# Kernel optimization log

Measured on AMD Instinct MI355X. Metric: run time of the kernel, lower is better.

Reference implementation:

```python
import jax, jax.numpy as jnp
import numpy as np

TANH_EPS = 1e-06
LOG2PI = float(np.log(2.0 * np.pi))


def _atanh(x):
    x = jnp.clip(x, -1.0 + TANH_EPS, 1.0 - TANH_EPS)
    return 0.5 * (jnp.log1p(x) - jnp.log1p(-x))


def setup_inputs() -> dict:
    key = jax.random.key(0)
    ks = jax.random.split(key, 12)
    T, B, O, H, A = 256, 1024, 128, 128, 8
    s = 0.05
    return {
        "obs_seq": jax.random.normal(ks[0], (T, B, O), jnp.float32),
        "actions_seq": jax.random.uniform(ks[1], (T, B, A), jnp.float32, -0.99, 0.99),
        "dones_seq": (jax.random.uniform(ks[2], (T, B)) < 0.02).astype(jnp.float32),
        "h0": jnp.zeros((B, H), jnp.float32),
        "c0": jnp.zeros((B, H), jnp.float32),
        "enc_w1": s * jax.random.normal(ks[3], (H, O), jnp.float32),
        "enc_b1": jnp.zeros((H,), jnp.float32),
        "enc_w2": s * jax.random.normal(ks[4], (H, H), jnp.float32),
        "enc_b2": jnp.zeros((H,), jnp.float32),
        "w_ih": s * jax.random.normal(ks[5], (4 * H, H), jnp.float32),
        "w_hh": s * jax.random.normal(ks[6], (4 * H, H), jnp.float32),
        "b_ih": jnp.zeros((4 * H,), jnp.float32),
        "b_hh": jnp.zeros((4 * H,), jnp.float32),
        "am_w": 0.01 * jax.random.normal(ks[7], (A, H), jnp.float32),
        "am_b": jnp.zeros((A,), jnp.float32),
        "actor_logstd": jnp.zeros((A,), jnp.float32),
        "cr_w": s * jax.random.normal(ks[8], (1, H), jnp.float32),
        "cr_b": jnp.zeros((1,), jnp.float32),
    }


def reference(obs_seq, actions_seq, dones_seq, h0, c0,
              enc_w1, enc_b1, enc_w2, enc_b2,
              w_ih, w_hh, b_ih, b_hh,
              am_w, am_b, actor_logstd, cr_w, cr_b):
    # Encoder (batched over all timesteps): two tanh MLP layers.
    x = jnp.tanh(jnp.einsum('tbo,ho->tbh', obs_seq, enc_w1) + enc_b1)
    x = jnp.tanh(jnp.einsum('tbh,gh->tbg', x, enc_w2) + enc_b2)
    # Precompute input contribution to gates: [T, B, 4H]
    xg = jnp.einsum('tbh,gh->tbg', x, w_ih) + b_ih

    def step(carry, inp):
        h, c = carry
        xg_t, d_t = inp
        m = (1.0 - d_t)[:, None]  # done-masking reset
        h = h * m
        c = c * m
        g = xg_t + h @ w_hh.T + b_hh
        i, f, gg, o = jnp.split(g, 4, axis=-1)
        c2 = jax.nn.sigmoid(f) * c + jax.nn.sigmoid(i) * jnp.tanh(gg)
        h2 = jax.nn.sigmoid(o) * jnp.tanh(c2)
        return (h2, c2), h2

    (hT, cT), ys = jax.lax.scan(step, (h0, c0), (xg, dones_seq))  # ys: [T, B, H]

    values = (jnp.einsum('tbh,vh->tbv', ys, cr_w) + cr_b)[..., 0]  # [T, B]
    mean = jnp.einsum('tbh,ah->tba', ys, am_w) + am_b  # [T, B, A]
    logstd = actor_logstd  # [A]
    u = _atanh(actions_seq)
    # Normal log-prob per dim, summed over action dims
    z = (u - mean) * jnp.exp(-logstd)
    lp_gauss = jnp.sum(-0.5 * z * z - logstd - 0.5 * LOG2PI, axis=-1)
    log_jac = jnp.sum(jnp.log(1.0 - actions_seq ** 2 + TANH_EPS), axis=-1)
    logprobs = lp_gauss - log_jac
    entropies = jnp.sum(0.5 + 0.5 * LOG2PI + logstd) + log_jac
    return logprobs, entropies, values, hT, cT
```

## Files before the change

### kernel.cpp

```cpp
#include <hip/hip_runtime.h>

typedef float f32x4 __attribute__((ext_vector_type(4)));
typedef short short8 __attribute__((ext_vector_type(8)));
typedef short s16x4 __attribute__((ext_vector_type(4)));

#define MFMA16(a, b, c) __builtin_amdgcn_mfma_f32_16x16x32_bf16((a), (b), (c), 0, 0, 0)

#define T_ 256
#define B_ 1024
#define H_ 128
#define TB_ 262144
#define BH_ 131072
#define LOG2PI_F 1.8378770664093453f

__device__ inline short f2bf(float f) {
    unsigned u = __builtin_bit_cast(unsigned, f);
    u += 0x7fffu + ((u >> 16) & 1u);
    return (short)(u >> 16);
}
__device__ inline float fexp(float x) { return __builtin_amdgcn_exp2f(x * 1.4426950408889634f); }
__device__ inline float fsigm(float x) { return __builtin_amdgcn_rcpf(1.f + fexp(-x)); }
__device__ inline float ftanh(float x) { return 1.f - 2.f * __builtin_amdgcn_rcpf(fexp(2.f * x) + 1.f); }

__device__ inline short8 pack8(float4 u0, float4 u1) {
    short8 p;
    p[0] = f2bf(u0.x); p[1] = f2bf(u0.y); p[2] = f2bf(u0.z); p[3] = f2bf(u0.w);
    p[4] = f2bf(u1.x); p[5] = f2bf(u1.y); p[6] = f2bf(u1.z); p[7] = f2bf(u1.w);
    return p;
}

__global__ __launch_bounds__(512, 4) void ex_kernel(
    const float* __restrict__ obs, const float* __restrict__ eb1,
    const float* __restrict__ eb2,
    const float* __restrict__ w1f, const float* __restrict__ w2f,
    short* __restrict__ x2p)
{
    __shared__ __align__(16) short xtA[64 * 128];
    __shared__ __align__(16) short xtB[64 * 128];
    __shared__ __align__(16) short xtC[64 * 128];
    const int tid = threadIdx.x;
    const int l = tid & 63, w = tid >> 6;
    const int l15 = l & 15, kg = l >> 4;
    const int srow = tid >> 3, sln = tid & 7;
    const int ssw = (srow & 7) << 3;

    short8 fw1[4], fw2[4];
#pragma unroll
    for (int kk = 0; kk < 4; ++kk) {
        const float* s1 = w1f + (w * 16 + l15) * 128 + kk * 32 + 8 * kg;
        const float* s2 = w2f + (w * 16 + l15) * 128 + kk * 32 + 8 * kg;
        fw1[kk] = pack8(*(const float4*)s1, *(const float4*)(s1 + 4));
        fw2[kk] = pack8(*(const float4*)s2, *(const float4*)(s2 + 4));
        asm volatile("" : "+v"(fw1[kk]), "+v"(fw2[kk]));
    }
    const float bb1 = eb1[w * 16 + l15], bb2 = eb2[w * 16 + l15];

    const int NT = 8;
    const int t0 = blockIdx.x * NT;

    {
        const float* src = obs + ((size_t)t0 * 64 + srow) * 128 + sln * 16;
#pragma unroll
        for (int ii = 0; ii < 2; ++ii) {
            float4 v0 = *(const float4*)(src + ii * 8);
            float4 v1 = *(const float4*)(src + ii * 8 + 4);
            *(short8*)(xtA + srow * 128 + ((sln * 16 + ii * 8) ^ ssw)) = pack8(v0, v1);
        }
    }
    __syncthreads();

    for (int i = 0; i < NT; ++i) {
        const int tile = t0 + i;
        short* bufO = (i & 1) ? xtB : xtA;
        short* bufN = (i & 1) ? xtA : xtB;

        float4 pf[4];
        {
            const int tn = (i + 1 < NT) ? tile + 1 : tile;
            const float* src = obs + ((size_t)tn * 64 + srow) * 128 + sln * 16;
#pragma unroll
            for (int ii = 0; ii < 4; ++ii) pf[ii] = *(const float4*)(src + ii * 4);
        }

#pragma unroll
        for (int mf = 0; mf < 4; ++mf) {
            const int ra = mf * 16 + l15, swa = (ra & 7) << 3;
            short8 a[4];
#pragma unroll
            for (int kk = 0; kk < 4; ++kk)
                a[kk] = *(const short8*)&bufO[ra * 128 + ((kk * 32 + 8 * kg) ^ swa)];
            f32x4 acc = {bb1, bb1, bb1, bb1};
#pragma unroll
            for (int kk = 0; kk < 4; ++kk) acc = MFMA16(a[kk], fw1[kk], acc);
#pragma unroll
            for (int j = 0; j < 4; ++j) {
                int rw = mf * 16 + kg * 4 + j;
                xtC[rw * 128 + ((w * 16 + l15) ^ ((rw & 7) << 3))] = f2bf(ftanh(acc[j]));
            }
        }
        __syncthreads();

        const int t = (tile * 64) >> 10;
        const int b_base = (tile * 64) & 1023;
#pragma unroll
        for (int mf = 0; mf < 4; ++mf) {
            const int ra = mf * 16 + l15, swa = (ra & 7) << 3;
            short8 a[4];
#pragma unroll
            for (int kk = 0; kk < 4; ++kk)
                a[kk] = *(const short8*)&xtC[ra * 128 + ((kk * 32 + 8 * kg) ^ swa)];
            f32x4 acc = {bb2, bb2, bb2, bb2};
#pragma unroll
            for (int kk = 0; kk < 4; ++kk) acc = MFMA16(a[kk], fw2[kk], acc);
#pragma unroll
            for (int j = 0; j < 4; ++j) {
                int b = b_base + mf * 16 + kg * 4 + j;
                size_t idx = (((size_t)t * 256 + (b >> 2)) * 4 + (b & 3)) * 128 + w * 16 + l15;
                x2p[idx] = f2bf(ftanh(acc[j]));
            }
        }
#pragma unroll
        for (int ii = 0; ii < 2; ++ii) {
            *(short8*)(bufN + srow * 128 + ((sln * 16 + ii * 8) ^ ssw)) =
                pack8(pf[ii * 2], pf[ii * 2 + 1]);
        }
        __syncthreads();
    }
}

__global__ __launch_bounds__(512) void lstm_kernel(
    const short* __restrict__ x2p, const float* __restrict__ whh,
    const float* __restrict__ wih,
    const float* __restrict__ h0, const float* __restrict__ c0,
    const float* __restrict__ bhh, const float* __restrict__ bih,
    const float* __restrict__ dones,
    const float* __restrict__ amw, const float* __restrict__ crw,
    const float* __restrict__ amb, const float* __restrict__ crb,
    float* __restrict__ headbuf, float* __restrict__ out)
{
    __shared__ __align__(16) short hbuf[2][4 * 160];
    __shared__ __align__(16) short hring[16 * 640];
    __shared__ __align__(16) short x2b[2][16 * 160];
    __shared__ float dlds[1028];
    const int tid = threadIdx.x;
    const int l = tid & 63, w = tid >> 6;
    const int l15 = l & 15, kg = l >> 4;
    const int b0 = blockIdx.x * 4;
    const int d = w * 16 + l15;
    const int blk = blockIdx.x;
    const int xsw = (l15 & 7) << 3;

    short8 bfr[4][4], bfi[4][4];
#pragma unroll
    for (int s = 0; s < 4; ++s)
#pragma unroll
        for (int kk = 0; kk < 4; ++kk) {
            const float* sr = whh + ((s * 128 + d) * 128 + kk * 32 + 8 * kg);
            const float* si = wih + ((s * 128 + d) * 128 + kk * 32 + 8 * kg);
            bfr[s][kk] = pack8(*(const float4*)sr, *(const float4*)(sr + 4));
            bfi[s][kk] = pack8(*(const float4*)si, *(const float4*)(si + 4));
            asm volatile("" : "+v"(bfr[s][kk]), "+v"(bfi[s][kk]));
        }

    short8 hb4[4];
#pragma unroll
    for (int kk = 0; kk < 4; ++kk) {
        if (l15 == 0) {
            const float* s0 = crw + kk * 32 + 8 * kg;
            hb4[kk] = pack8(*(const float4*)s0, *(const float4*)(s0 + 4));
        } else if (l15 <= 8) {
            const float* s0 = amw + (l15 - 1) * 128 + kk * 32 + 8 * kg;
            hb4[kk] = pack8(*(const float4*)s0, *(const float4*)(s0 + 4));
        } else {
            hb4[kk] = short8{0, 0, 0, 0, 0, 0, 0, 0};
        }
        asm volatile("" : "+v"(hb4[kk]));
    }
    const float biasH = (l15 == 0) ? crb[0] : (l15 <= 8 ? amb[l15 - 1] : 0.f);

    for (int i = tid; i < 1028; i += 512) {
        int t = i >> 2, jj = i & 3;
        dlds[i] = (t < 256) ? 1.f - dones[t * 1024 + b0 + jj] : 1.f;
    }

    float bh[4];
#pragma unroll
    for (int s = 0; s < 4; ++s) bh[s] = bhh[s * 128 + d] + bih[s * 128 + d];

    const int st_toff = tid >> 7, st_j = (tid >> 5) & 3, st_dim = (tid & 31) * 4;
    const int st_row = st_j * 4 + st_toff;
    const int xrow160 = st_row * 160 + (st_dim ^ ((st_row & 7) << 3));
#define X2GIDX(G) ((((size_t)(((G) * 4 + st_toff) <= 255 ? ((G) * 4 + st_toff) : 255) * 256 + blk) * 4 + st_j) * 128 + st_dim)

    {
        s16x4 v0 = *(const s16x4*)(x2p + X2GIDX(0));
        s16x4 v1 = *(const s16x4*)(x2p + X2GIDX(1));
        *(s16x4*)&x2b[0][xrow160] = v0;
        *(s16x4*)&x2b[1][xrow160] = v1;
    }
    s16x4 xpf = *(const s16x4*)(x2p + X2GIDX(2));
    asm volatile("s_waitcnt lgkmcnt(0)" ::: "memory");
    __syncthreads();

    f32x4 xgA[4], xgB[4];
#pragma unroll
    for (int s = 0; s < 4; ++s) {
        short8 ax[4];
#pragma unroll
        for (int kk = 0; kk < 4; ++kk)
            ax[kk] = *(const short8*)&x2b[0][l15 * 160 + ((kk * 32 + kg * 8) ^ xsw)];
        f32x4 accX = {bh[s], bh[s], bh[s], bh[s]};
#pragma unroll
        for (int kk = 0; kk < 4; ++kk) accX = MFMA16(ax[kk], bfi[s][kk], accX);
        xgA[s] = accX;
    }

    float h = h0[(b0 + kg) * 128 + d];
    float c = c0[(b0 + kg) * 128 + d];
    hbuf[0][kg * 160 + d] = f2bf(h * dlds[kg]);
    asm volatile("s_waitcnt lgkmcnt(0)" ::: "memory");
    __syncthreads();

    const int aoff = (l15 >> 2) * 160;
    float mreg = dlds[kg];

#define LSTM_STEP(t, hb, i_s, xgC, xgN, x2R, DO_T3, GNEXT, DO_HEAD)                        \
    {                                                                                      \
        short8 a[4];                                                                       \
        _Pragma("unroll")                                                                  \
        for (int kk = 0; kk < 4; ++kk)                                                     \
            a[kk] = *(const short8*)&hbuf[hb][aoff + kk * 32 + kg * 8];                    \
        f32x4 acc[4];                                                                      \
        _Pragma("unroll")                                                                  \
        for (int s = 0; s < 4; ++s) acc[s] = xgC[s];                                       \
        _Pragma("unroll")                                                                  \
        for (int kk = 0; kk < 4; ++kk)                                                     \
            _Pragma("unroll")                                                              \
            for (int s = 0; s < 4; ++s) acc[s] = MFMA16(a[kk], bfr[s][kk], acc[s]);        \
        {           \
            short8 ax[4];                                                                  \
            _Pragma("unroll")                                                              \
            for (int kk = 0; kk < 4; ++kk)                                                 \
                ax[kk] = *(const short8*)&x2R[l15 * 160 + ((kk * 32 + kg * 8) ^ xsw)];     \
            f32x4 accX = {bh[i_s], bh[i_s], bh[i_s], bh[i_s]};                             \
            _Pragma("unroll")                                                              \
            for (int kk = 0; kk < 4; ++kk) accX = MFMA16(ax[kk], bfi[i_s][kk], accX);      \
            xgN[i_s] = accX;                                                               \
        }                                                                                  \
        if (DO_HEAD) {                 \
            int th = (t) - 8 + w;                                                          \
            const short* hr = &hring[(th & 15) * 640];                                     \
            short8 ah[4];                                                                  \
            _Pragma("unroll")                                                              \
            for (int kk = 0; kk < 4; ++kk)                                                 \
                ah[kk] = *(const short8*)&hr[aoff + kk * 32 + kg * 8];                     \
            f32x4 aH = {biasH, biasH, biasH, biasH};                                       \
            _Pragma("unroll")                                                              \
            for (int kk = 0; kk < 4; ++kk) aH = MFMA16(ah[kk], hb4[kk], aH);               \
            if (l15 < 9) headbuf[(th * 1024 + b0 + kg) * 12 + l15] = aH[0];                \
        }                                                                                  \
        if (DO_T3) {                                                                      \
            *(s16x4*)&x2W[xrow160] = xpf;                                                  \
            xpf = *(const s16x4*)(x2p + X2GIDX(GNEXT));                                    \
        }                                                                                  \
        float mn = dlds[((t) + 1) * 4 + kg];                                               \
        float gi = acc[0][i_s];                                                            \
        float gf = acc[1][i_s];                                                            \
        float gg = acc[2][i_s];                                                            \
        float go = acc[3][i_s];                                                            \
        c = fsigm(gf) * (c * mreg) + fsigm(gi) * ftanh(gg);                                \
        float h2 = fsigm(go) * ftanh(c);                                                   \
        h = h2;                                                                            \
        mreg = mn;                                                                         \
        hbuf[(hb) ^ 1][kg * 160 + d] = f2bf(h2 * mn);                                      \
        hring[((t) & 15) * 640 + kg * 160 + d] = f2bf(h2);                                 \
        asm volatile("s_waitcnt lgkmcnt(0)" ::: "memory");                                 \
        __builtin_amdgcn_s_barrier();                                                      \
        asm volatile("" ::: "memory");                                                     \
    }

    for (int g = 0; g < 64; g += 2) {
        {
            const int tb = g * 4;
            const short* x2R = &x2b[1][0];
            short* x2W = &x2b[0][0];
            LSTM_STEP(tb + 0, 0, 0, xgA, xgB, x2R, 0, 0, (g > 0));
            LSTM_STEP(tb + 1, 1, 1, xgA, xgB, x2R, 0, 0, 0);
            LSTM_STEP(tb + 2, 0, 2, xgA, xgB, x2R, 0, 0, 0);
            LSTM_STEP(tb + 3, 1, 3, xgA, xgB, x2R, 1, (g + 3), 0);
        }
        {
            const int tb = (g + 1) * 4;
            const short* x2R = &x2b[0][0];
            short* x2W = &x2b[1][0];
            LSTM_STEP(tb + 0, 0, 0, xgB, xgA, x2R, 0, 0, 0);
            LSTM_STEP(tb + 1, 1, 1, xgB, xgA, x2R, 0, 0, 0);
            LSTM_STEP(tb + 2, 0, 2, xgB, xgA, x2R, 0, 0, 0);
            LSTM_STEP(tb + 3, 1, 3, xgB, xgA, x2R, 1, (g + 4), 0);
        }
    }
#undef LSTM_STEP
#undef X2GIDX

    {
        int th = 248 + w;
        const short* hr = &hring[(th & 15) * 640];
        short8 ah[4];
#pragma unroll
        for (int kk = 0; kk < 4; ++kk)
            ah[kk] = *(const short8*)&hr[aoff + kk * 32 + kg * 8];
        f32x4 aH = {biasH, biasH, biasH, biasH};
#pragma unroll
        for (int kk = 0; kk < 4; ++kk) aH = MFMA16(ah[kk], hb4[kk], aH);
        if (l15 < 9) headbuf[(th * 1024 + b0 + kg) * 12 + l15] = aH[0];
    }

    out[3 * TB_ + (b0 + kg) * 128 + d] = h;
    out[3 * TB_ + BH_ + (b0 + kg) * 128 + d] = c;
}

__global__ __launch_bounds__(256) void headepi_kernel(
    const float* __restrict__ headbuf, const float* __restrict__ lstd,
    const float* __restrict__ actions, float* __restrict__ out)
{
    const int r = blockIdx.x * 256 + threadIdx.x;
    const float* hp = headbuf + (size_t)r * 12;
    float4 m0 = *(const float4*)(hp);
    float4 m1 = *(const float4*)(hp + 4);
    float4 m2 = *(const float4*)(hp + 8);
    const float* ap = actions + (size_t)r * 8;
    float4 a0 = *(const float4*)(ap);
    float4 a1 = *(const float4*)(ap + 4);
    float mean[8] = {m0.y, m0.z, m0.w, m1.x, m1.y, m1.z, m1.w, m2.x};
    float act[8] = {a0.x, a0.y, a0.z, a0.w, a1.x, a1.y, a1.z, a1.w};
    float lp = 0.f, lj = 0.f, entS = 0.f;
#pragma unroll
    for (int ai = 0; ai < 8; ++ai) {
        float x = act[ai];
        float xc = fminf(fmaxf(x, -1.f + 1e-6f), 1.f - 1e-6f);
        float u = 0.5f * logf((1.f + xc) / (1.f - xc));
        float ls = lstd[ai];
        float z = (u - mean[ai]) * expf(-ls);
        lp += -0.5f * z * z - ls;
        lj += logf(1.f - x * x + 1e-6f);
        entS += ls;
    }
    lp -= 8.f * 0.5f * LOG2PI_F;
    entS += 8.f * (0.5f + 0.5f * LOG2PI_F);
    out[r] = lp - lj;
    out[TB_ + r] = entS + lj;
    out[2 * TB_ + r] = m0.x;
}

extern "C" void kernel_launch(void* const* d_in, const int* in_sizes, int n_in,
                              void* d_out, int out_size, void* d_ws, size_t ws_size,
                              hipStream_t stream) {
    const float* obs   = (const float*)d_in[0];
    const float* acts  = (const float*)d_in[1];
    const float* dones = (const float*)d_in[2];
    const float* h0    = (const float*)d_in[3];
    const float* c0    = (const float*)d_in[4];
    const float* w1    = (const float*)d_in[5];
    const float* b1    = (const float*)d_in[6];
    const float* w2    = (const float*)d_in[7];
    const float* b2    = (const float*)d_in[8];
    const float* wih   = (const float*)d_in[9];
    const float* whh   = (const float*)d_in[10];
    const float* bih   = (const float*)d_in[11];
    const float* bhh   = (const float*)d_in[12];
    const float* amw   = (const float*)d_in[13];
    const float* amb   = (const float*)d_in[14];
    const float* lstd  = (const float*)d_in[15];
    const float* crw   = (const float*)d_in[16];
    const float* crb   = (const float*)d_in[17];
    float* out = (float*)d_out;

    char* ws = (char*)d_ws;
    short* x2p = (short*)(ws);
    float* hbf = (float*)(ws + 67108864);
    if (ws_size < (size_t)67108864 + 12582912) return;

    hipLaunchKernelGGL(ex_kernel, dim3(512), dim3(512), 0, stream,
                       obs, b1, b2, w1, w2, x2p);
    hipLaunchKernelGGL(lstm_kernel, dim3(256), dim3(512), 0, stream,
                       x2p, whh, wih, h0, c0, bhh, bih, dones, amw, crw, amb, crb, hbf, out);
    hipLaunchKernelGGL(headepi_kernel, dim3(1024), dim3(256), 0, stream,
                       hbf, lstd, acts, out);
}
```

Baseline: 216.2 us.

## Fuse observation encoder into recurrent LSTM kernel, dropping the separate encoder pass

The two-layer tanh encoder no longer runs as its own kernel. Each LSTM block now loads obs for its 4 batch rows, runs both encoder layers with weights held in LDS, and spreads that work across the per-step schedule (stage obs, layer 1, layer 2 on separate steps). This removes the separate launch and the bf16 x2 round trip through global memory. In exchange each step of the latency-bound recurrent loop carries extra LDS traffic and MFMA work, the head computation is offset by a different step lag, and LDS use grows by 64KB of encoder weights per block.

```diff
diff --git a/kernel.cpp b/kernel.cpp
--- a/kernel.cpp
+++ b/kernel.cpp
@@ -29,126 +29,66 @@
     return p;
 }
 
-__global__ __launch_bounds__(512, 4) void ex_kernel(
-    const float* __restrict__ obs, const float* __restrict__ eb1,
-    const float* __restrict__ eb2,
-    const float* __restrict__ w1f, const float* __restrict__ w2f,
-    short* __restrict__ x2p)
+__device__ __forceinline__ void enc_layer(
+    const short* inb, const short* wL, float bias, short* outb,
+    int l15, int kg, int w)
 {
-    __shared__ __align__(16) short xtA[64 * 128];
-    __shared__ __align__(16) short xtB[64 * 128];
-    __shared__ __align__(16) short xtC[64 * 128];
-    const int tid = threadIdx.x;
-    const int l = tid & 63, w = tid >> 6;
-    const int l15 = l & 15, kg = l >> 4;
-    const int srow = tid >> 3, sln = tid & 7;
-    const int ssw = (srow & 7) << 3;
-
-    short8 fw1[4], fw2[4];
+    const int xsw = (l15 & 7) << 3;
+    const int wr = w * 16 + l15, wsw = (wr & 7) << 3;
+    short8 a[4], b[4];
 #pragma unroll
     for (int kk = 0; kk < 4; ++kk) {
-        const float* s1 = w1f + (w * 16 + l15) * 128 + kk * 32 + 8 * kg;
-        const float* s2 = w2f + (w * 16 + l15) * 128 + kk * 32 + 8 * kg;
-        fw1[kk] = pack8(*(const float4*)s1, *(const float4*)(s1 + 4));
-        fw2[kk] = pack8(*(const float4*)s2, *(const float4*)(s2 + 4));
-        asm volatile("" : "+v"(fw1[kk]), "+v"(fw2[kk]));
-    }
-    const float bb1 = eb1[w * 16 + l15], bb2 = eb2[w * 16 + l15];
-
-    const int NT = 8;
-    const int t0 = blockIdx.x * NT;
-
-    {
-        const float* src = obs + ((size_t)t0 * 64 + srow) * 128 + sln * 16;
-#pragma unroll
-        for (int ii = 0; ii < 2; ++ii) {
-            float4 v0 = *(const float4*)(src + ii * 8);
-            float4 v1 = *(const float4*)(src + ii * 8 + 4);
-            *(short8*)(xtA + srow * 128 + ((sln * 16 + ii * 8) ^ ssw)) = pack8(v0, v1);
-        }
-    }
-    __syncthreads();
-
-    for (int i = 0; i < NT; ++i) {
-        const int tile = t0 + i;
-        short* bufO = (i & 1) ? xtB : xtA;
-        short* bufN = (i & 1) ? xtA : xtB;
-
-        float4 pf[4];
-        {
-            const int tn = (i + 1 < NT) ? tile + 1 : tile;
-            const float* src = obs + ((size_t)tn * 64 + srow) * 128 + sln * 16;
-#pragma unroll
-            for (int ii = 0; ii < 4; ++ii) pf[ii] = *(const float4*)(src + ii * 4);
-        }
-
-#pragma unroll
-        for (int mf = 0; mf < 4; ++mf) {
-            const int ra = mf * 16 + l15, swa = (ra & 7) << 3;
-            short8 a[4];
-#pragma unroll
-            for (int kk = 0; kk < 4; ++kk)
-                a[kk] = *(const short8*)&bufO[ra * 128 + ((kk * 32 + 8 * kg) ^ swa)];
-            f32x4 acc = {bb1, bb1, bb1, bb1};
-#pragma unroll
-            for (int kk = 0; kk < 4; ++kk) acc = MFMA16(a[kk], fw1[kk], acc);
-#pragma unroll
-            for (int j = 0; j < 4; ++j) {
-                int rw = mf * 16 + kg * 4 + j;
-                xtC[rw * 128 + ((w * 16 + l15) ^ ((rw & 7) << 3))] = f2bf(ftanh(acc[j]));
-            }
-        }
-        __syncthreads();
-
-        const int t = (tile * 64) >> 10;
-        const int b_base = (tile * 64) & 1023;
-#pragma unroll
-        for (int mf = 0; mf < 4; ++mf) {
-            const int ra = mf * 16 + l15, swa = (ra & 7) << 3;
-            short8 a[4];
-#pragma unroll
-            for (int kk = 0; kk < 4; ++kk)
-                a[kk] = *(const short8*)&xtC[ra * 128 + ((kk * 32 + 8 * kg) ^ swa)];
-            f32x4 acc = {bb2, bb2, bb2, bb2};
-#pragma unroll
-            for (int kk = 0; kk < 4; ++kk) acc = MFMA16(a[kk], fw2[kk], acc);
-#pragma unroll
-            for (int j = 0; j < 4; ++j) {
-                int b = b_base + mf * 16 + kg * 4 + j;
-                size_t idx = (((size_t)t * 256 + (b >> 2)) * 4 + (b & 3)) * 128 + w * 16 + l15;
-                x2p[idx] = f2bf(ftanh(acc[j]));
-            }
-        }
-#pragma unroll
-        for (int ii = 0; ii < 2; ++ii) {
-            *(short8*)(bufN + srow * 128 + ((sln * 16 + ii * 8) ^ ssw)) =
-                pack8(pf[ii * 2], pf[ii * 2 + 1]);
-        }
-        __syncthreads();
+        a[kk] = *(const short8*)&inb[l15 * 160 + ((kk * 32 + kg * 8) ^ xsw)];
+        b[kk] = *(const short8*)&wL[wr * 128 + ((kk * 32 + kg * 8) ^ wsw)];
+    }
+    f32x4 acc = {bias, bias, bias, bias};
+#pragma unroll
+    for (int kk = 0; kk < 4; ++kk) acc = MFMA16(a[kk], b[kk], acc);
+#pragma unroll
+    for (int j = 0; j < 4; ++j) {
+        const int row = kg * 4 + j;
+        outb[row * 160 + (wr ^ ((row & 7) << 3))] = f2bf(ftanh(acc[j]));
     }
 }
 
 __global__ __launch_bounds__(512) void lstm_kernel(
-    const short* __restrict__ x2p, const float* __restrict__ whh,
-    const float* __restrict__ wih,
+    const float* __restrict__ obs,
+    const float* __restrict__ whh, const float* __restrict__ wih,
     const float* __restrict__ h0, const float* __restrict__ c0,
     const float* __restrict__ bhh, const float* __restrict__ bih,
     const float* __restrict__ dones,
     const float* __restrict__ amw, const float* __restrict__ crw,
     const float* __restrict__ amb, const float* __restrict__ crb,
+    const float* __restrict__ w1f, const float* __restrict__ eb1,
+    const float* __restrict__ w2f, const float* __restrict__ eb2,
     float* __restrict__ headbuf, float* __restrict__ out)
 {
+    __shared__ __align__(16) short w1L[128 * 128];
+    __shared__ __align__(16) short w2L[128 * 128];
+    __shared__ __align__(16) short obsb[16 * 160];
+    __shared__ __align__(16) short x1b[16 * 160];
+    __shared__ __align__(16) short x2b[2][16 * 160];
     __shared__ __align__(16) short hbuf[2][4 * 160];
     __shared__ __align__(16) short hring[16 * 640];
-    __shared__ __align__(16) short x2b[2][16 * 160];
     __shared__ float dlds[1028];
     const int tid = threadIdx.x;
     const int l = tid & 63, w = tid >> 6;
     const int l15 = l & 15, kg = l >> 4;
     const int b0 = blockIdx.x * 4;
     const int d = w * 16 + l15;
-    const int blk = blockIdx.x;
     const int xsw = (l15 & 7) << 3;
+
+    for (int idx = tid * 4; idx < 16384; idx += 2048) {
+        const int row = idx >> 7, db = idx & 127;
+        float4 v1 = *(const float4*)(w1f + idx);
+        float4 v2 = *(const float4*)(w2f + idx);
+        s16x4 p1, p2;
+        p1[0] = f2bf(v1.x); p1[1] = f2bf(v1.y); p1[2] = f2bf(v1.z); p1[3] = f2bf(v1.w);
+        p2[0] = f2bf(v2.x); p2[1] = f2bf(v2.y); p2[2] = f2bf(v2.z); p2[3] = f2bf(v2.w);
+        const int sa = row * 128 + (db ^ ((row & 7) << 3));
+        *(s16x4*)&w1L[sa] = p1;
+        *(s16x4*)&w2L[sa] = p2;
+    }
 
     short8 bfr[4][4], bfi[4][4];
 #pragma unroll
@@ -177,6 +117,7 @@
         asm volatile("" : "+v"(hb4[kk]));
     }
     const float biasH = (l15 == 0) ? crb[0] : (l15 <= 8 ? amb[l15 - 1] : 0.f);
+    const float bb1 = eb1[d], bb2 = eb2[d];
 
     for (int i = tid; i < 1028; i += 512) {
         int t = i >> 2, jj = i & 3;
@@ -187,20 +128,36 @@
 #pragma unroll
     for (int s = 0; s < 4; ++s) bh[s] = bhh[s * 128 + d] + bih[s * 128 + d];
 
-    const int st_toff = tid >> 7, st_j = (tid >> 5) & 3, st_dim = (tid & 31) * 4;
-    const int st_row = st_j * 4 + st_toff;
-    const int xrow160 = st_row * 160 + (st_dim ^ ((st_row & 7) << 3));
-#define X2GIDX(G) ((((size_t)(((G) * 4 + st_toff) <= 255 ? ((G) * 4 + st_toff) : 255) * 256 + blk) * 4 + st_j) * 128 + st_dim)
+    const int ob_toff = (tid >> 5) & 3, ob_j = tid >> 7, ob_dim = (tid & 31) * 4;
+    const int ob_row = ob_j * 4 + ob_toff;
+    const int ob_lds = ob_row * 160 + (ob_dim ^ ((ob_row & 7) << 3));
+#define OBSIDX(G) ((((size_t)(((G) * 4 + ob_toff) <= 255 ? ((G) * 4 + ob_toff) : 255)) * 1024 + b0 + ob_j) * 128 + ob_dim)
+#define STAGE_OBS(V)                                                                       \
+    {                                                                                      \
+        s16x4 p;                                                                           \
+        p[0] = f2bf((V).x); p[1] = f2bf((V).y); p[2] = f2bf((V).z); p[3] = f2bf((V).w);    \
+        *(s16x4*)&obsb[ob_lds] = p;                                                        \
+    }
 
     {
-        s16x4 v0 = *(const s16x4*)(x2p + X2GIDX(0));
-        s16x4 v1 = *(const s16x4*)(x2p + X2GIDX(1));
-        *(s16x4*)&x2b[0][xrow160] = v0;
-        *(s16x4*)&x2b[1][xrow160] = v1;
-    }
-    s16x4 xpf = *(const s16x4*)(x2p + X2GIDX(2));
-    asm volatile("s_waitcnt lgkmcnt(0)" ::: "memory");
-    __syncthreads();
+        float4 v = *(const float4*)(obs + OBSIDX(0));
+        STAGE_OBS(v);
+    }
+    __syncthreads();
+    enc_layer(obsb, w1L, bb1, x1b, l15, kg, w);
+    __syncthreads();
+    enc_layer(x1b, w2L, bb2, &x2b[0][0], l15, kg, w);
+    __syncthreads();
+    {
+        float4 v = *(const float4*)(obs + OBSIDX(1));
+        STAGE_OBS(v);
+    }
+    __syncthreads();
+    enc_layer(obsb, w1L, bb1, x1b, l15, kg, w);
+    __syncthreads();
+    enc_layer(x1b, w2L, bb2, &x2b[1][0], l15, kg, w);
+    __syncthreads();
+    float4 opf = *(const float4*)(obs + OBSIDX(2));
 
     f32x4 xgA[4], xgB[4];
 #pragma unroll
@@ -224,8 +181,12 @@
     const int aoff = (l15 >> 2) * 160;
     float mreg = dlds[kg];
 
-#define LSTM_STEP(t, hb, i_s, xgC, xgN, x2R, DO_T3, GNEXT, DO_HEAD)                        \
+#define LSTM_STEP(t, hb, i_s, xgC, xgN, x2R, DO_STAGE, GNEXT, DO_L1, DO_L2, DO_HEAD)       \
     {                                                                                      \
+        if (DO_STAGE) {                                                                    \
+            STAGE_OBS(opf);                                                                \
+            opf = *(const float4*)(obs + OBSIDX(GNEXT));                                   \
+        }                                                                                  \
         short8 a[4];                                                                       \
         _Pragma("unroll")                                                                  \
         for (int kk = 0; kk < 4; ++kk)                                                     \
@@ -247,8 +208,10 @@
             for (int kk = 0; kk < 4; ++kk) accX = MFMA16(ax[kk], bfi[i_s][kk], accX);      \
             xgN[i_s] = accX;                                                               \
         }                                                                                  \
-        if (DO_HEAD) {                 \
-            int th = (t) - 8 + w;                                                          \
+        if (DO_L1) enc_layer(obsb, w1L, bb1, x1b, l15, kg, w);                             \
+        if (DO_L2) enc_layer(x1b, w2L, bb2, x2W, l15, kg, w);                              \
+        if (DO_HEAD) {                \
+            int th = (t) - 11 + w;                                                         \
             const short* hr = &hring[(th & 15) * 640];                                     \
             short8 ah[4];                                                                  \
             _Pragma("unroll")                                                              \
@@ -258,10 +221,6 @@
             _Pragma("unroll")                                                              \
             for (int kk = 0; kk < 4; ++kk) aH = MFMA16(ah[kk], hb4[kk], aH);               \
             if (l15 < 9) headbuf[(th * 1024 + b0 + kg) * 12 + l15] = aH[0];                \
-        }                                                                                  \
-        if (DO_T3) {                                                                      \
-            *(s16x4*)&x2W[xrow160] = xpf;                                                  \
-            xpf = *(const s16x4*)(x2p + X2GIDX(GNEXT));                                    \
         }                                                                                  \
         float mn = dlds[((t) + 1) * 4 + kg];                                               \
         float gi = acc[0][i_s];                                                            \
@@ -284,23 +243,24 @@
             const int tb = g * 4;
             const short* x2R = &x2b[1][0];
             short* x2W = &x2b[0][0];
-            LSTM_STEP(tb + 0, 0, 0, xgA, xgB, x2R, 0, 0, (g > 0));
-            LSTM_STEP(tb + 1, 1, 1, xgA, xgB, x2R, 0, 0, 0);
-            LSTM_STEP(tb + 2, 0, 2, xgA, xgB, x2R, 0, 0, 0);
-            LSTM_STEP(tb + 3, 1, 3, xgA, xgB, x2R, 1, (g + 3), 0);
+            LSTM_STEP(tb + 0, 0, 0, xgA, xgB, x2R, 1, (g + 3), 0, 0, 0);
+            LSTM_STEP(tb + 1, 1, 1, xgA, xgB, x2R, 0, 0, 1, 0, 0);
+            LSTM_STEP(tb + 2, 0, 2, xgA, xgB, x2R, 0, 0, 0, 1, 0);
+            LSTM_STEP(tb + 3, 1, 3, xgA, xgB, x2R, 0, 0, 0, 0, (g > 0));
         }
         {
             const int tb = (g + 1) * 4;
             const short* x2R = &x2b[0][0];
             short* x2W = &x2b[1][0];
-            LSTM_STEP(tb + 0, 0, 0, xgB, xgA, x2R, 0, 0, 0);
-            LSTM_STEP(tb + 1, 1, 1, xgB, xgA, x2R, 0, 0, 0);
-            LSTM_STEP(tb + 2, 0, 2, xgB, xgA, x2R, 0, 0, 0);
-            LSTM_STEP(tb + 3, 1, 3, xgB, xgA, x2R, 1, (g + 4), 0);
+            LSTM_STEP(tb + 0, 0, 0, xgB, xgA, x2R, 1, (g + 4), 0, 0, 0);
+            LSTM_STEP(tb + 1, 1, 1, xgB, xgA, x2R, 0, 0, 1, 0, 0);
+            LSTM_STEP(tb + 2, 0, 2, xgB, xgA, x2R, 0, 0, 0, 1, 0);
+            LSTM_STEP(tb + 3, 1, 3, xgB, xgA, x2R, 0, 0, 0, 0, 0);
         }
     }
 #undef LSTM_STEP
-#undef X2GIDX
+#undef STAGE_OBS
+#undef OBSIDX
 
     {
         int th = 248 + w;
@@ -375,15 +335,12 @@
     const float* crb   = (const float*)d_in[17];
     float* out = (float*)d_out;
 
-    char* ws = (char*)d_ws;
-    short* x2p = (short*)(ws);
-    float* hbf = (float*)(ws + 67108864);
-    if (ws_size < (size_t)67108864 + 12582912) return;
-
-    hipLaunchKernelGGL(ex_kernel, dim3(512), dim3(512), 0, stream,
-                       obs, b1, b2, w1, w2, x2p);
+    float* hbf = (float*)d_ws;
+    if (ws_size < (size_t)12582912) return;
+
     hipLaunchKernelGGL(lstm_kernel, dim3(256), dim3(512), 0, stream,
-                       x2p, whh, wih, h0, c0, bhh, bih, dones, amw, crw, amb, crb, hbf, out);
+                       obs, whh, wih, h0, c0, bhh, bih, dones,
+                       amw, crw, amb, crb, w1, b1, w2, b2, hbf, out);
     hipLaunchKernelGGL(headepi_kernel, dim3(1024), dim3(256), 0, stream,
                        hbf, lstd, acts, out);
 }
```

After: 270.9 us. 25.3% more time.
